# Performance work log

Measured on AMD Instinct MI355X. Metric: run time of the kernel, lower is better.

Reference implementation:

```python
import jax, jax.numpy as jnp
import numpy as np

N = 100000   # nodes
E = 1600000  # edges
D = 128      # in_dim
H = 128      # hidden_dim
C = 40       # num_classes
EPS = 1e-5   # LayerNorm eps (torch default)


def setup_inputs() -> dict:
    key = jax.random.key(0)
    ks = jax.random.split(key, 16)
    x = jax.random.normal(ks[0], (N, D), dtype=jnp.float32)
    edge_index = jax.random.randint(ks[1], (2, E), 0, N, dtype=jnp.int64)
    s = 1.0 / np.sqrt(D)
    inp = {"x": x, "edge_index": edge_index}
    # 3 GCN layers: weight [in, H], bias [H]; LayerNorm gamma/beta [H]
    for i in range(3):
        inp[f"W{i}"] = jax.random.normal(ks[2 + i], (D if i == 0 else H, H), dtype=jnp.float32) * s
        inp[f"b{i}"] = jnp.zeros((H,), jnp.float32)
        inp[f"g{i}"] = jnp.ones((H,), jnp.float32)
        inp[f"be{i}"] = jnp.zeros((H,), jnp.float32)
    inp["Wc"] = jax.random.normal(ks[10], (H, C), dtype=jnp.float32) * (1.0 / np.sqrt(H))
    inp["bc"] = jnp.zeros((C,), jnp.float32)
    return inp


def _layer_norm(h, g, b):
    mu = jnp.mean(h, axis=-1, keepdims=True)
    var = jnp.var(h, axis=-1, keepdims=True)  # biased, matches torch
    return (h - mu) * jax.lax.rsqrt(var + EPS) * g + b


def _gcn_conv(x, W, b, src, dst, enorm, dinv2):
    # GCNConv: D^{-1/2}(A+I)D^{-1/2} X W + b (self-loops handled analytically)
    h = x @ W                                   # [N, H]
    agg = jax.ops.segment_sum(h[src] * enorm[:, None], dst, num_segments=N)
    return agg + h * dinv2[:, None] + b


def reference(x, edge_index, W0, b0, g0, be0, W1, b1, g1, be1, W2, b2, g2, be2, Wc, bc):
    src, dst = edge_index[0], edge_index[1]
    # degree with self-loops (GCNConv adds self-loops by default)
    deg = jnp.zeros((N,), x.dtype).at[dst].add(1.0) + 1.0
    dinv = jax.lax.rsqrt(deg)
    enorm = dinv[src] * dinv[dst]               # per-edge normalization
    dinv2 = dinv * dinv                         # self-loop normalization

    Ws, bs, gs, bes = (W0, W1, W2), (b0, b1, b2), (g0, g1, g2), (be0, be1, be2)
    for i in range(3):
        x_in = x
        x = _gcn_conv(x, Ws[i], bs[i], src, dst, enorm, dinv2)
        x = _layer_norm(x, gs[i], bes[i])
        x = jax.nn.elu(x)
        if i > 0:
            x = x + x_in
        # dropout: eval mode / p=0 -> identity
    return x @ Wc + bc
```

## Files before the change

kernel.cpp:

```cpp
#include <hip/hip_runtime.h>
#include <math.h>

#define N_NODES 100000
#define N_EDGES 1600000
#define DIM     128
#define NCLS    40
#define NBUCK   196
#define P1_CH   4096
#define P1_GRID 391

typedef _Float16 f16x8 __attribute__((ext_vector_type(8)));
typedef _Float16 f16x2 __attribute__((ext_vector_type(2)));
typedef float    f32x4 __attribute__((ext_vector_type(4)));

__device__ inline unsigned short f16bits(float f) {
    union { _Float16 h; unsigned short u; } cv;
    cv.h = (_Float16)f;
    return cv.u;
}
__device__ inline f16x2 as_h2(unsigned u) {
    union { unsigned u; f16x2 h; } cv;
    cv.u = u;
    return cv.h;
}
__device__ inline unsigned as_u(f16x2 h) {
    union { f16x2 h; unsigned u; } cv;
    cv.h = h;
    return cv.u;
}
__device__ inline unsigned pack_h2(float lo, float hi) {
    f16x2 h;
    h.x = (_Float16)lo;
    h.y = (_Float16)hi;
    return as_u(h);
}
__device__ inline int wave_incl_scan(int v, int lane) {
#pragma unroll
    for (int off = 1; off < 64; off <<= 1) {
        int x = __shfl_up(v, off, 64);
        if (lane >= off) v += x;
    }
    return v;
}

__global__ __launch_bounds__(256) void setup_misc(const float* __restrict__ W0,
                                                  const float* __restrict__ W1,
                                                  const float* __restrict__ W2,
                                                  const float* __restrict__ Wc,
                                                  const int* __restrict__ ei,
                                                  unsigned short* __restrict__ Wsw0,
                                                  unsigned short* __restrict__ Wsw1,
                                                  unsigned short* __restrict__ Wsw2,
                                                  unsigned short* __restrict__ Wcsw,
                                                  int* __restrict__ bcnt) {
    int blk = blockIdx.x;
    if (blk < 192) {
        const float* W = (blk < 64) ? W0 : (blk < 128) ? W1 : W2;
        unsigned short* Wsw = (blk < 64) ? Wsw0 : (blk < 128) ? Wsw1 : Wsw2;
        int o = (blk & 63) * 256 + threadIdx.x;
        int f = o >> 9;
        int l = (o >> 3) & 63;
        int j = o & 7;
        int n = f >> 2;
        int s = f & 3;
        int k = s * 32 + (l >> 4) * 8 + j;
        int c = (l & 15) * 8 + n;
        Wsw[o] = f16bits(W[k * DIM + c]);
    } else if (blk < 216) {
        int o = (blk - 192) * 256 + threadIdx.x;
        int f = o >> 9;
        int l = (o >> 3) & 63;
        int j = o & 7;
        int n = f >> 2;
        int s = f & 3;
        int k = s * 32 + (l >> 4) * 8 + j;
        int c = (l & 15) * 3 + n;
        Wcsw[o] = (c < NCLS) ? f16bits(Wc[k * NCLS + c]) : (unsigned short)0;
    } else {
        __shared__ int h[256];
        const int t  = threadIdx.x;
        const int e0 = (blk - 216) * P1_CH;
        const int cnt = min(P1_CH, N_EDGES - e0);
        h[t] = 0;
        __syncthreads();
        for (int i = t; i < cnt; i += 256)
            atomicAdd(&h[ei[N_EDGES + e0 + i] >> 9], 1);
        __syncthreads();
        if (h[t]) atomicAdd(&bcnt[t], h[t]);
    }
}

__global__ __launch_bounds__(256) void bucket_p1(const int* __restrict__ ei,
                                                 const int* __restrict__ bcnt,
                                                 int* __restrict__ boff,
                                                 unsigned* __restrict__ tmp) {
    __shared__ int  hist[256];
    __shared__ int  lscan[256];
    __shared__ int  rank[256];
    __shared__ int  gbase[256];
    __shared__ int  wtotA[4];
    __shared__ int  wtotB[4];
    __shared__ int2 stage[P1_CH];
    const int t  = threadIdx.x;
    const int lane = t & 63, wv = t >> 6;
    const int e0 = blockIdx.x * P1_CH;
    const int cnt = min(P1_CH, N_EDGES - e0);

    int bcv = (t < NBUCK) ? bcnt[t] : 0;

    hist[t] = 0;
    __syncthreads();

    int2 ed[16];
#pragma unroll
    for (int i = 0; i < 16; ++i) {
        int idx = t + i * 256;
        if (idx < cnt) {
            int s = ei[e0 + idx];
            int d = ei[N_EDGES + e0 + idx];
            ed[i] = make_int2(s, d);
            atomicAdd(&hist[d >> 9], 1);
        }
    }
    __syncthreads();

    int hv = hist[t];
    int inclA = hv, inclB = bcv;
#pragma unroll
    for (int off = 1; off < 64; off <<= 1) {
        int xa = __shfl_up(inclA, off, 64);
        int xb = __shfl_up(inclB, off, 64);
        if (lane >= off) { inclA += xa; inclB += xb; }
    }
    if (lane == 63) { wtotA[wv] = inclA; wtotB[wv] = inclB; }
    __syncthreads();
    int pA = 0, pB = 0;
    for (int i = 0; i < wv; ++i) { pA += wtotA[i]; pB += wtotB[i]; }
    inclA += pA;
    inclB += pB;
    int exclA = inclA - hv;
    int exclB = inclB - bcv;
    lscan[t] = exclA;
    rank[t]  = exclA;
    if (hv > 0) gbase[t] = exclB + atomicAdd(&boff[t], hv);
    __syncthreads();

#pragma unroll
    for (int i = 0; i < 16; ++i) {
        int idx = t + i * 256;
        if (idx < cnt) {
            int b = ed[i].y >> 9;
            int p = atomicAdd(&rank[b], 1);
            stage[p] = ed[i];
        }
    }
    __syncthreads();

    for (int p = t; p < cnt; p += 256) {
        int2 v = stage[p];
        int b = v.y >> 9;
        tmp[gbase[b] + (p - lscan[b])] = ((unsigned)v.x << 9) | ((unsigned)v.y & 511u);
    }
}

__global__ __launch_bounds__(256) void bucket_p2(const unsigned* __restrict__ tmp,
                                                 const int* __restrict__ bcnt,
                                                 int* __restrict__ rowptr,
                                                 float* __restrict__ dinv,
                                                 unsigned* __restrict__ rec) {
    __shared__ int cnt[512];
    __shared__ int cur[512];
    __shared__ int wtot[4];
    __shared__ int sbeg, send;
    const int t  = threadIdx.x;
    const int lane = t & 63, wv = t >> 6;
    const int b  = blockIdx.x;
    const int d0 = b << 9;
    const int dend = min(d0 + 512, N_NODES);
    const int nn = dend - d0;

    int bcv = (t < NBUCK) ? bcnt[t] : 0;
    int binc = wave_incl_scan(bcv, lane);
    if (lane == 63) wtot[wv] = binc;
    cnt[t] = 0;
    cnt[t + 256] = 0;
    __syncthreads();
    {
        int pfx = 0;
        for (int i = 0; i < wv; ++i) pfx += wtot[i];
        binc += pfx;
        if (t == b) { sbeg = binc - bcv; send = binc; }
    }
    __syncthreads();

    const int beg = sbeg;
    const int end = send;
    for (int idx = beg + t; idx < end; idx += 256)
        atomicAdd(&cnt[tmp[idx] & 511u], 1);
    __syncthreads();

    int c0 = cnt[2 * t];
    int c1 = cnt[2 * t + 1];
    int pv = c0 + c1;
    int incl = wave_incl_scan(pv, lane);
    if (lane == 63) wtot[wv] = incl;
    __syncthreads();
    int prefix = 0;
    for (int i = 0; i < wv; ++i) prefix += wtot[i];
    incl += prefix;
    int excl = incl - pv;
    int base0 = beg + excl;
    int base1 = base0 + c0;
    cur[2 * t]     = base0;
    cur[2 * t + 1] = base1;
    if (2 * t < nn) {
        rowptr[d0 + 2 * t] = base0;
        dinv[d0 + 2 * t]   = rsqrtf((float)c0 + 1.0f);
    }
    if (2 * t + 1 < nn) {
        rowptr[d0 + 2 * t + 1] = base1;
        dinv[d0 + 2 * t + 1]   = rsqrtf((float)c1 + 1.0f);
    }
    if (b == NBUCK - 1 && t == 0) rowptr[N_NODES] = N_EDGES;
    __syncthreads();

    for (int idx = beg + t; idx < end; idx += 256) {
        unsigned u = tmp[idx];
        int pos = atomicAdd(&cur[u & 511u], 1);
        rec[pos] = (u >> 9) << 8;
    }
}

__global__ __launch_bounds__(256) void gemm_mfma_f(const float* __restrict__ X,
                                                   const unsigned short* __restrict__ Wsw,
                                                   const float* __restrict__ dinv,
                                                   unsigned short* __restrict__ H) {
    __shared__ unsigned short wlds[32 * 512];
    const int tid   = threadIdx.x;
    const int lane  = tid & 63;
    const int wave  = tid >> 6;
    const int row0w = blockIdx.x * 64 + wave * 16;
    const int m = lane & 15;
    const int q = lane >> 4;

    {
        const uint4* srcp = (const uint4*)Wsw;
        uint4*       dstp = (uint4*)wlds;
#pragma unroll
        for (int i = 0; i < 8; ++i) dstp[tid + i * 256] = srcp[tid + i * 256];
    }
    __syncthreads();

    int r = row0w + m;
    if (r >= N_NODES) r = N_NODES - 1;
    const float* xp = X + (size_t)r * DIM + q * 8;
    f16x8 af[4];
#pragma unroll
    for (int s = 0; s < 4; ++s) {
        float4 x0 = *(const float4*)(xp + s * 32);
        float4 x1 = *(const float4*)(xp + s * 32 + 4);
        f16x8 v;
        v[0] = (_Float16)x0.x; v[1] = (_Float16)x0.y;
        v[2] = (_Float16)x0.z; v[3] = (_Float16)x0.w;
        v[4] = (_Float16)x1.x; v[5] = (_Float16)x1.y;
        v[6] = (_Float16)x1.z; v[7] = (_Float16)x1.w;
        af[s] = v;
    }

    f32x4 acc[8];
    f32x4 z = {0.f, 0.f, 0.f, 0.f};
#pragma unroll
    for (int n = 0; n < 8; ++n) acc[n] = z;

    const unsigned short* wl = wlds + lane * 8;
#pragma unroll
    for (int s = 0; s < 4; ++s)
#pragma unroll
        for (int n = 0; n < 8; ++n) {
            f16x8 wf = *(const f16x8*)(wl + ((n * 4 + s) << 9));
            acc[n] = __builtin_amdgcn_mfma_f32_16x16x32_f16(af[s], wf, acc[n], 0, 0, 0);
        }

#pragma unroll
    for (int j = 0; j < 4; ++j) {
        int row = row0w + q * 4 + j;
        if (row < N_NODES) {
            float dv = dinv[row];
            uint4 o;
            o.x = pack_h2(acc[0][j] * dv, acc[1][j] * dv);
            o.y = pack_h2(acc[2][j] * dv, acc[3][j] * dv);
            o.z = pack_h2(acc[4][j] * dv, acc[5][j] * dv);
            o.w = pack_h2(acc[6][j] * dv, acc[7][j] * dv);
            *(uint4*)(H + (size_t)row * DIM + m * 8) = o;
        } else {
            uint4 zz = make_uint4(0u, 0u, 0u, 0u);
            *(uint4*)(H + (size_t)row * DIM + m * 8) = zz;
        }
    }
}

__global__ __launch_bounds__(256) void gemm_mfma_h(const unsigned short* __restrict__ Xh,
                                                   const unsigned short* __restrict__ Wsw,
                                                   const float* __restrict__ dinv,
                                                   unsigned short* __restrict__ H) {
    __shared__ unsigned short wlds[32 * 512];
    const int tid   = threadIdx.x;
    const int lane  = tid & 63;
    const int wave  = tid >> 6;
    const int row0w = blockIdx.x * 64 + wave * 16;
    const int m = lane & 15;
    const int q = lane >> 4;

    {
        const uint4* srcp = (const uint4*)Wsw;
        uint4*       dstp = (uint4*)wlds;
#pragma unroll
        for (int i = 0; i < 8; ++i) dstp[tid + i * 256] = srcp[tid + i * 256];
    }
    __syncthreads();

    int r = row0w + m;
    if (r >= N_NODES) r = N_NODES - 1;
    const unsigned short* xp = Xh + (size_t)r * DIM + q * 8;
    f16x8 af[4];
#pragma unroll
    for (int s = 0; s < 4; ++s) af[s] = *(const f16x8*)(xp + s * 32);

    f32x4 acc[8];
    f32x4 z = {0.f, 0.f, 0.f, 0.f};
#pragma unroll
    for (int n = 0; n < 8; ++n) acc[n] = z;

    const unsigned short* wl = wlds + lane * 8;
#pragma unroll
    for (int s = 0; s < 4; ++s)
#pragma unroll
        for (int n = 0; n < 8; ++n) {
            f16x8 wf = *(const f16x8*)(wl + ((n * 4 + s) << 9));
            acc[n] = __builtin_amdgcn_mfma_f32_16x16x32_f16(af[s], wf, acc[n], 0, 0, 0);
        }

#pragma unroll
    for (int j = 0; j < 4; ++j) {
        int row = row0w + q * 4 + j;
        if (row < N_NODES) {
            float dv = dinv[row];
            uint4 o;
            o.x = pack_h2(acc[0][j] * dv, acc[1][j] * dv);
            o.y = pack_h2(acc[2][j] * dv, acc[3][j] * dv);
            o.z = pack_h2(acc[4][j] * dv, acc[5][j] * dv);
            o.w = pack_h2(acc[6][j] * dv, acc[7][j] * dv);
            *(uint4*)(H + (size_t)row * DIM + m * 8) = o;
        } else {
            uint4 zz = make_uint4(0u, 0u, 0u, 0u);
            *(uint4*)(H + (size_t)row * DIM + m * 8) = zz;
        }
    }
}

__global__ __launch_bounds__(256) void agg_ln(const unsigned short* __restrict__ Hh,
                                              const unsigned short* __restrict__ xin,
                                              const float* __restrict__ dinv,
                                              const float* __restrict__ bias,
                                              const float* __restrict__ g,
                                              const float* __restrict__ be,
                                              const int* __restrict__ rowptr,
                                              const unsigned* __restrict__ rec,
                                              unsigned short* __restrict__ outb) {
    const int tid  = threadIdx.x;
    const int lane = tid & 63;
    const int l16  = tid & 15;
    const int gb   = lane & 48;
    const int node = blockIdx.x * 16 + (tid >> 4);
    const int beg  = rowptr[node];
    const int end  = rowptr[node + 1];
    const char* Hb8 = (const char*)Hh;
    const unsigned laneoff = (unsigned)l16 * 16;
    const unsigned sentin  = (unsigned)N_NODES << 8;

    f16x2 accA[4], accB[4], accC[4], accD[4];
    f16x2 hz = {(_Float16)0.f, (_Float16)0.f};
#pragma unroll
    for (int k = 0; k < 4; ++k) { accA[k] = hz; accB[k] = hz; accC[k] = hz; accD[k] = hz; }

    for (int e0 = beg; e0 < end; e0 += 16) {
        int cnt = min(end - e0, 16);
        unsigned sv = (l16 < cnt) ? rec[e0 + l16] : sentin;
        int cntR = (cnt + 7) & ~7;
        for (int j = 0; j < cntR; j += 8) {
            unsigned o0 = (unsigned)__shfl((int)sv, gb + j + 0, 64) + laneoff;
            unsigned o1 = (unsigned)__shfl((int)sv, gb + j + 1, 64) + laneoff;
            unsigned o2 = (unsigned)__shfl((int)sv, gb + j + 2, 64) + laneoff;
            unsigned o3 = (unsigned)__shfl((int)sv, gb + j + 3, 64) + laneoff;
            unsigned o4 = (unsigned)__shfl((int)sv, gb + j + 4, 64) + laneoff;
            unsigned o5 = (unsigned)__shfl((int)sv, gb + j + 5, 64) + laneoff;
            unsigned o6 = (unsigned)__shfl((int)sv, gb + j + 6, 64) + laneoff;
            unsigned o7 = (unsigned)__shfl((int)sv, gb + j + 7, 64) + laneoff;
            uint4 u0 = *(const uint4*)(Hb8 + o0);
            uint4 u1 = *(const uint4*)(Hb8 + o1);
            uint4 u2 = *(const uint4*)(Hb8 + o2);
            uint4 u3 = *(const uint4*)(Hb8 + o3);
            uint4 u4 = *(const uint4*)(Hb8 + o4);
            uint4 u5 = *(const uint4*)(Hb8 + o5);
            uint4 u6 = *(const uint4*)(Hb8 + o6);
            uint4 u7 = *(const uint4*)(Hb8 + o7);
            accA[0] += as_h2(u0.x); accA[1] += as_h2(u0.y); accA[2] += as_h2(u0.z); accA[3] += as_h2(u0.w);
            accB[0] += as_h2(u1.x); accB[1] += as_h2(u1.y); accB[2] += as_h2(u1.z); accB[3] += as_h2(u1.w);
            accC[0] += as_h2(u2.x); accC[1] += as_h2(u2.y); accC[2] += as_h2(u2.z); accC[3] += as_h2(u2.w);
            accD[0] += as_h2(u3.x); accD[1] += as_h2(u3.y); accD[2] += as_h2(u3.z); accD[3] += as_h2(u3.w);
            accA[0] += as_h2(u4.x); accA[1] += as_h2(u4.y); accA[2] += as_h2(u4.z); accA[3] += as_h2(u4.w);
            accB[0] += as_h2(u5.x); accB[1] += as_h2(u5.y); accB[2] += as_h2(u5.z); accB[3] += as_h2(u5.w);
            accC[0] += as_h2(u6.x); accC[1] += as_h2(u6.y); accC[2] += as_h2(u6.z); accC[3] += as_h2(u6.w);
            accD[0] += as_h2(u7.x); accD[1] += as_h2(u7.y); accD[2] += as_h2(u7.z); accD[3] += as_h2(u7.w);
        }
    }

#pragma unroll
    for (int k = 0; k < 4; ++k) accA[k] = (accA[k] + accB[k]) + (accC[k] + accD[k]);

    const float dv = dinv[node];
    const unsigned nodeoff = ((unsigned)node << 8) + laneoff;
    uint4 hv = *(const uint4*)(Hb8 + nodeoff);
    const int c0 = l16 * 8;
    float4 bb0 = *(const float4*)(bias + c0);
    float4 bb1 = *(const float4*)(bias + c0 + 4);
    f16x2 h0 = as_h2(hv.x), h1 = as_h2(hv.y), h2 = as_h2(hv.z), h3 = as_h2(hv.w);

    float a[8];
    a[0] = ((float)accA[0].x + (float)h0.x) * dv + bb0.x;
    a[1] = ((float)accA[0].y + (float)h0.y) * dv + bb0.y;
    a[2] = ((float)accA[1].x + (float)h1.x) * dv + bb0.z;
    a[3] = ((float)accA[1].y + (float)h1.y) * dv + bb0.w;
    a[4] = ((float)accA[2].x + (float)h2.x) * dv + bb1.x;
    a[5] = ((float)accA[2].y + (float)h2.y) * dv + bb1.y;
    a[6] = ((float)accA[3].x + (float)h3.x) * dv + bb1.z;
    a[7] = ((float)accA[3].y + (float)h3.y) * dv + bb1.w;

    float s1 = 0.f, s2 = 0.f;
#pragma unroll
    for (int i = 0; i < 8; ++i) { s1 += a[i]; s2 += a[i] * a[i]; }
#pragma unroll
    for (int mk = 1; mk <= 8; mk <<= 1) {
        s1 += __shfl_xor(s1, mk, 64);
        s2 += __shfl_xor(s2, mk, 64);
    }
    float mean = s1 * (1.0f / 128.0f);
    float var  = s2 * (1.0f / 128.0f) - mean * mean;
    float rr   = rsqrtf(var + 1e-5f);

    float4 gg0 = *(const float4*)(g + c0);
    float4 gg1 = *(const float4*)(g + c0 + 4);
    float4 ee0 = *(const float4*)(be + c0);
    float4 ee1 = *(const float4*)(be + c0 + 4);

    float r[8];
    r[0] = (a[0] - mean) * rr * gg0.x + ee0.x;
    r[1] = (a[1] - mean) * rr * gg0.y + ee0.y;
    r[2] = (a[2] - mean) * rr * gg0.z + ee0.z;
    r[3] = (a[3] - mean) * rr * gg0.w + ee0.w;
    r[4] = (a[4] - mean) * rr * gg1.x + ee1.x;
    r[5] = (a[5] - mean) * rr * gg1.y + ee1.y;
    r[6] = (a[6] - mean) * rr * gg1.z + ee1.z;
    r[7] = (a[7] - mean) * rr * gg1.w + ee1.w;
#pragma unroll
    for (int i = 0; i < 8; ++i) r[i] = r[i] > 0.0f ? r[i] : expm1f(r[i]);

    if (xin) {
        uint4 xv = *(const uint4*)((const char*)xin + nodeoff);
        f16x2 x0 = as_h2(xv.x), x1 = as_h2(xv.y), x2 = as_h2(xv.z), x3 = as_h2(xv.w);
        r[0] += (float)x0.x; r[1] += (float)x0.y;
        r[2] += (float)x1.x; r[3] += (float)x1.y;
        r[4] += (float)x2.x; r[5] += (float)x2.y;
        r[6] += (float)x3.x; r[7] += (float)x3.y;
    }

    uint4 o;
    o.x = pack_h2(r[0], r[1]);
    o.y = pack_h2(r[2], r[3]);
    o.z = pack_h2(r[4], r[5]);
    o.w = pack_h2(r[6], r[7]);
    *(uint4*)((char*)outb + nodeoff) = o;
}

__global__ __launch_bounds__(256) void agg_ln_cls(const unsigned short* __restrict__ Hh,
                                                  const unsigned short* __restrict__ xin,
                                                  const float* __restrict__ dinv,
                                                  const float* __restrict__ bias,
                                                  const float* __restrict__ g,
                                                  const float* __restrict__ be,
                                                  const int* __restrict__ rowptr,
                                                  const unsigned* __restrict__ rec,
                                                  const unsigned short* __restrict__ Wcsw,
                                                  const float* __restrict__ bc,
                                                  float* __restrict__ out) {
    __shared__ _Float16 hl[16][136];
    const int tid  = threadIdx.x;
    const int lane = tid & 63;
    const int l16  = tid & 15;
    const int gb   = lane & 48;
    const int grp  = tid >> 4;
    const int node0 = blockIdx.x * 16;
    const int node = node0 + grp;
    const int beg  = rowptr[node];
    const int end  = rowptr[node + 1];
    const char* Hb8 = (const char*)Hh;
    const unsigned laneoff = (unsigned)l16 * 16;
    const unsigned sentin  = (unsigned)N_NODES << 8;

    f16x2 accA[4], accB[4], accC[4], accD[4];
    f16x2 hz = {(_Float16)0.f, (_Float16)0.f};
#pragma unroll
    for (int k = 0; k < 4; ++k) { accA[k] = hz; accB[k] = hz; accC[k] = hz; accD[k] = hz; }

    for (int e0 = beg; e0 < end; e0 += 16) {
        int cnt = min(end - e0, 16);
        unsigned sv = (l16 < cnt) ? rec[e0 + l16] : sentin;
        int cntR = (cnt + 7) & ~7;
        for (int j = 0; j < cntR; j += 8) {
            unsigned o0 = (unsigned)__shfl((int)sv, gb + j + 0, 64) + laneoff;
            unsigned o1 = (unsigned)__shfl((int)sv, gb + j + 1, 64) + laneoff;
            unsigned o2 = (unsigned)__shfl((int)sv, gb + j + 2, 64) + laneoff;
            unsigned o3 = (unsigned)__shfl((int)sv, gb + j + 3, 64) + laneoff;
            unsigned o4 = (unsigned)__shfl((int)sv, gb + j + 4, 64) + laneoff;
            unsigned o5 = (unsigned)__shfl((int)sv, gb + j + 5, 64) + laneoff;
            unsigned o6 = (unsigned)__shfl((int)sv, gb + j + 6, 64) + laneoff;
            unsigned o7 = (unsigned)__shfl((int)sv, gb + j + 7, 64) + laneoff;
            uint4 u0 = *(const uint4*)(Hb8 + o0);
            uint4 u1 = *(const uint4*)(Hb8 + o1);
            uint4 u2 = *(const uint4*)(Hb8 + o2);
            uint4 u3 = *(const uint4*)(Hb8 + o3);
            uint4 u4 = *(const uint4*)(Hb8 + o4);
            uint4 u5 = *(const uint4*)(Hb8 + o5);
            uint4 u6 = *(const uint4*)(Hb8 + o6);
            uint4 u7 = *(const uint4*)(Hb8 + o7);
            accA[0] += as_h2(u0.x); accA[1] += as_h2(u0.y); accA[2] += as_h2(u0.z); accA[3] += as_h2(u0.w);
            accB[0] += as_h2(u1.x); accB[1] += as_h2(u1.y); accB[2] += as_h2(u1.z); accB[3] += as_h2(u1.w);
            accC[0] += as_h2(u2.x); accC[1] += as_h2(u2.y); accC[2] += as_h2(u2.z); accC[3] += as_h2(u2.w);
            accD[0] += as_h2(u3.x); accD[1] += as_h2(u3.y); accD[2] += as_h2(u3.z); accD[3] += as_h2(u3.w);
            accA[0] += as_h2(u4.x); accA[1] += as_h2(u4.y); accA[2] += as_h2(u4.z); accA[3] += as_h2(u4.w);
            accB[0] += as_h2(u5.x); accB[1] += as_h2(u5.y); accB[2] += as_h2(u5.z); accB[3] += as_h2(u5.w);
            accC[0] += as_h2(u6.x); accC[1] += as_h2(u6.y); accC[2] += as_h2(u6.z); accC[3] += as_h2(u6.w);
            accD[0] += as_h2(u7.x); accD[1] += as_h2(u7.y); accD[2] += as_h2(u7.z); accD[3] += as_h2(u7.w);
        }
    }

#pragma unroll
    for (int k = 0; k < 4; ++k) accA[k] = (accA[k] + accB[k]) + (accC[k] + accD[k]);

    const float dv = dinv[node];
    const unsigned nodeoff = ((unsigned)node << 8) + laneoff;
    uint4 hv = *(const uint4*)(Hb8 + nodeoff);
    const int c0 = l16 * 8;
    float4 bb0 = *(const float4*)(bias + c0);
    float4 bb1 = *(const float4*)(bias + c0 + 4);
    f16x2 h0 = as_h2(hv.x), h1 = as_h2(hv.y), h2 = as_h2(hv.z), h3 = as_h2(hv.w);

    float a[8];
    a[0] = ((float)accA[0].x + (float)h0.x) * dv + bb0.x;
    a[1] = ((float)accA[0].y + (float)h0.y) * dv + bb0.y;
    a[2] = ((float)accA[1].x + (float)h1.x) * dv + bb0.z;
    a[3] = ((float)accA[1].y + (float)h1.y) * dv + bb0.w;
    a[4] = ((float)accA[2].x + (float)h2.x) * dv + bb1.x;
    a[5] = ((float)accA[2].y + (float)h2.y) * dv + bb1.y;
    a[6] = ((float)accA[3].x + (float)h3.x) * dv + bb1.z;
    a[7] = ((float)accA[3].y + (float)h3.y) * dv + bb1.w;

    float s1 = 0.f, s2 = 0.f;
#pragma unroll
    for (int i = 0; i < 8; ++i) { s1 += a[i]; s2 += a[i] * a[i]; }
#pragma unroll
    for (int mk = 1; mk <= 8; mk <<= 1) {
        s1 += __shfl_xor(s1, mk, 64);
        s2 += __shfl_xor(s2, mk, 64);
    }
    float mean = s1 * (1.0f / 128.0f);
    float var  = s2 * (1.0f / 128.0f) - mean * mean;
    float rr   = rsqrtf(var + 1e-5f);

    float4 gg0 = *(const float4*)(g + c0);
    float4 gg1 = *(const float4*)(g + c0 + 4);
    float4 ee0 = *(const float4*)(be + c0);
    float4 ee1 = *(const float4*)(be + c0 + 4);

    float r[8];
    r[0] = (a[0] - mean) * rr * gg0.x + ee0.x;
    r[1] = (a[1] - mean) * rr * gg0.y + ee0.y;
    r[2] = (a[2] - mean) * rr * gg0.z + ee0.z;
    r[3] = (a[3] - mean) * rr * gg0.w + ee0.w;
    r[4] = (a[4] - mean) * rr * gg1.x + ee1.x;
    r[5] = (a[5] - mean) * rr * gg1.y + ee1.y;
    r[6] = (a[6] - mean) * rr * gg1.z + ee1.z;
    r[7] = (a[7] - mean) * rr * gg1.w + ee1.w;
#pragma unroll
    for (int i = 0; i < 8; ++i) r[i] = r[i] > 0.0f ? r[i] : expm1f(r[i]);

    if (xin) {
        uint4 xv = *(const uint4*)((const char*)xin + nodeoff);
        f16x2 x0 = as_h2(xv.x), x1 = as_h2(xv.y), x2 = as_h2(xv.z), x3 = as_h2(xv.w);
        r[0] += (float)x0.x; r[1] += (float)x0.y;
        r[2] += (float)x1.x; r[3] += (float)x1.y;
        r[4] += (float)x2.x; r[5] += (float)x2.y;
        r[6] += (float)x3.x; r[7] += (float)x3.y;
    }

    uint4 o;
    o.x = pack_h2(r[0], r[1]);
    o.y = pack_h2(r[2], r[3]);
    o.z = pack_h2(r[4], r[5]);
    o.w = pack_h2(r[6], r[7]);
    *(uint4*)&hl[grp][l16 * 8] = o;
    __syncthreads();

    if (tid < 64) {
        const int m = lane & 15;
        const int q = lane >> 4;

        f16x8 wf[12];
#pragma unroll
        for (int f = 0; f < 12; ++f)
            wf[f] = *(const f16x8*)(Wcsw + (f << 9) + lane * 8);

        f16x8 af[4];
#pragma unroll
        for (int s = 0; s < 4; ++s)
            af[s] = *(const f16x8*)&hl[m][q * 8 + s * 32];

        f32x4 acc[3];
        f32x4 z = {0.f, 0.f, 0.f, 0.f};
#pragma unroll
        for (int n = 0; n < 3; ++n) acc[n] = z;

#pragma unroll
        for (int s = 0; s < 4; ++s)
#pragma unroll
            for (int n = 0; n < 3; ++n)
                acc[n] = __builtin_amdgcn_mfma_f32_16x16x32_f16(af[s], wf[n * 4 + s], acc[n], 0, 0, 0);

#pragma unroll
        for (int j = 0; j < 4; ++j) {
            int row = node0 + q * 4 + j;
#pragma unroll
            for (int n = 0; n < 3; ++n) {
                int c = 3 * m + n;
                if (c < NCLS)
                    out[(size_t)row * NCLS + c] = acc[n][j] + bc[c];
            }
        }
    }
}

extern "C" void kernel_launch(void* const* d_in, const int* in_sizes, int n_in,
                              void* d_out, int out_size, void* d_ws, size_t ws_size,
                              hipStream_t stream) {
    const float* x  = (const float*)d_in[0];
    const int*   ei = (const int*)d_in[1];
    const float* W[3]  = {(const float*)d_in[2], (const float*)d_in[6], (const float*)d_in[10]};
    const float* b[3]  = {(const float*)d_in[3], (const float*)d_in[7], (const float*)d_in[11]};
    const float* g[3]  = {(const float*)d_in[4], (const float*)d_in[8], (const float*)d_in[12]};
    const float* be[3] = {(const float*)d_in[5], (const float*)d_in[9], (const float*)d_in[13]};
    const float* Wc = (const float*)d_in[14];
    const float* bc = (const float*)d_in[15];
    float* out = (float*)d_out;

    char* ws = (char*)d_ws;
    const size_t NP = 400128;
    float* dinv   = (float*)(ws);
    int*   rowptr = (int*)  (ws + NP);
    int*   bcnt   = (int*)  (ws + 2 * NP);
    int*   boff   = (int*)  (ws + 2 * NP + 1024);
    unsigned* rec = (unsigned*)(ws + 2 * NP + 4096);
    unsigned short* Hh = (unsigned short*)(ws + 2 * NP + 4096 + (size_t)N_EDGES * 8);
    unsigned short* Ah = Hh + (size_t)(N_NODES + 64) * DIM;
    unsigned short* Ch = Ah + (size_t)N_NODES * DIM;
    unsigned short* Wsw0 = Ch + (size_t)N_NODES * DIM;
    unsigned short* Wsw1 = Wsw0 + DIM * DIM;
    unsigned short* Wsw2 = Wsw1 + DIM * DIM;
    unsigned short* Wcsw = Wsw2 + DIM * DIM;
    unsigned* tmp = (unsigned*)Ch;

    hipMemsetAsync(bcnt, 0, 2048, stream);
    setup_misc<<<216 + P1_GRID, 256, 0, stream>>>(W[0], W[1], W[2], Wc, ei,
                                                  Wsw0, Wsw1, Wsw2, Wcsw, bcnt);

    bucket_p1<<<P1_GRID, 256, 0, stream>>>(ei, bcnt, boff, tmp);
    bucket_p2<<<NBUCK, 256, 0, stream>>>(tmp, bcnt, rowptr, dinv, rec);

    const int gemm_grid = (N_NODES + 63) / 64;
    const int agg_grid  = N_NODES / 16;

    gemm_mfma_f<<<gemm_grid, 256, 0, stream>>>(x, Wsw0, dinv, Hh);
    agg_ln<<<agg_grid, 256, 0, stream>>>(Hh, nullptr, dinv, b[0], g[0], be[0], rowptr, rec, Ch);

    gemm_mfma_h<<<gemm_grid, 256, 0, stream>>>(Ch, Wsw1, dinv, Hh);
    agg_ln<<<agg_grid, 256, 0, stream>>>(Hh, Ch, dinv, b[1], g[1], be[1], rowptr, rec, Ah);

    gemm_mfma_h<<<gemm_grid, 256, 0, stream>>>(Ah, Wsw2, dinv, Hh);
    agg_ln_cls<<<agg_grid, 256, 0, stream>>>(Hh, Ah, dinv, b[2], g[2], be[2], rowptr, rec,
                                             Wcsw, bc, out);
}
```

Before: 389.4 us.

## Fuse next-layer GEMM into aggregation+LayerNorm kernel epilogue

Replaces the separate gemm_mfma_h launches by computing each block's 16 output rows times the next layer weight inside the aggregation kernel, via LDS staging and MFMA with weights read directly from global memory. The aim is to avoid re-reading the layer activations from HBM and to save two kernel launches. H is double-buffered (H1/H2) because aggregation gathers from arbitrary rows, and the padding rows of H2 are zeroed in setup. The residual input and the output buffer Ch are now aliased across the two fused layers, and each wave writes strided 4-byte stores, which could hurt coalescing.

Result: faster. 372.2 us (-4.4%).

```diff
diff --git a/kernel.cpp b/kernel.cpp
--- a/kernel.cpp
+++ b/kernel.cpp
@@ -52,7 +52,8 @@
                                                   unsigned short* __restrict__ Wsw1,
                                                   unsigned short* __restrict__ Wsw2,
                                                   unsigned short* __restrict__ Wcsw,
-                                                  int* __restrict__ bcnt) {
+                                                  int* __restrict__ bcnt,
+                                                  unsigned short* __restrict__ H2) {
     int blk = blockIdx.x;
     if (blk < 192) {
         const float* W = (blk < 64) ? W0 : (blk < 128) ? W1 : W2;
@@ -76,7 +77,7 @@
         int k = s * 32 + (l >> 4) * 8 + j;
         int c = (l & 15) * 3 + n;
         Wcsw[o] = (c < NCLS) ? f16bits(Wc[k * NCLS + c]) : (unsigned short)0;
-    } else {
+    } else if (blk < 216 + P1_GRID) {
         __shared__ int h[256];
         const int t  = threadIdx.x;
         const int e0 = (blk - 216) * P1_CH;
@@ -87,6 +88,11 @@
             atomicAdd(&h[ei[N_EDGES + e0 + i] >> 9], 1);
         __syncthreads();
         if (h[t]) atomicAdd(&bcnt[t], h[t]);
+    } else {
+        uint4* p = (uint4*)(H2 + (size_t)N_NODES * DIM);
+        uint4 zz = make_uint4(0u, 0u, 0u, 0u);
+#pragma unroll
+        for (int i = 0; i < 4; ++i) p[threadIdx.x + i * 256] = zz;
     }
 }
 
@@ -299,79 +305,26 @@
     }
 }
 
-__global__ __launch_bounds__(256) void gemm_mfma_h(const unsigned short* __restrict__ Xh,
+__global__ __launch_bounds__(256) void agg_ln_gemm(const unsigned short* __restrict__ Hh,
+                                                   const unsigned short* __restrict__ xin,
+                                                   const float* __restrict__ dinv,
+                                                   const float* __restrict__ bias,
+                                                   const float* __restrict__ g,
+                                                   const float* __restrict__ be,
+                                                   const int* __restrict__ rowptr,
+                                                   const unsigned* __restrict__ rec,
                                                    const unsigned short* __restrict__ Wsw,
-                                                   const float* __restrict__ dinv,
-                                                   unsigned short* __restrict__ H) {
-    __shared__ unsigned short wlds[32 * 512];
-    const int tid   = threadIdx.x;
-    const int lane  = tid & 63;
-    const int wave  = tid >> 6;
-    const int row0w = blockIdx.x * 64 + wave * 16;
-    const int m = lane & 15;
-    const int q = lane >> 4;
-
-    {
-        const uint4* srcp = (const uint4*)Wsw;
-        uint4*       dstp = (uint4*)wlds;
-#pragma unroll
-        for (int i = 0; i < 8; ++i) dstp[tid + i * 256] = srcp[tid + i * 256];
-    }
-    __syncthreads();
-
-    int r = row0w + m;
-    if (r >= N_NODES) r = N_NODES - 1;
-    const unsigned short* xp = Xh + (size_t)r * DIM + q * 8;
-    f16x8 af[4];
-#pragma unroll
-    for (int s = 0; s < 4; ++s) af[s] = *(const f16x8*)(xp + s * 32);
-
-    f32x4 acc[8];
-    f32x4 z = {0.f, 0.f, 0.f, 0.f};
-#pragma unroll
-    for (int n = 0; n < 8; ++n) acc[n] = z;
-
-    const unsigned short* wl = wlds + lane * 8;
-#pragma unroll
-    for (int s = 0; s < 4; ++s)
-#pragma unroll
-        for (int n = 0; n < 8; ++n) {
-            f16x8 wf = *(const f16x8*)(wl + ((n * 4 + s) << 9));
-            acc[n] = __builtin_amdgcn_mfma_f32_16x16x32_f16(af[s], wf, acc[n], 0, 0, 0);
-        }
-
-#pragma unroll
-    for (int j = 0; j < 4; ++j) {
-        int row = row0w + q * 4 + j;
-        if (row < N_NODES) {
-            float dv = dinv[row];
-            uint4 o;
-            o.x = pack_h2(acc[0][j] * dv, acc[1][j] * dv);
-            o.y = pack_h2(acc[2][j] * dv, acc[3][j] * dv);
-            o.z = pack_h2(acc[4][j] * dv, acc[5][j] * dv);
-            o.w = pack_h2(acc[6][j] * dv, acc[7][j] * dv);
-            *(uint4*)(H + (size_t)row * DIM + m * 8) = o;
-        } else {
-            uint4 zz = make_uint4(0u, 0u, 0u, 0u);
-            *(uint4*)(H + (size_t)row * DIM + m * 8) = zz;
-        }
-    }
-}
-
-__global__ __launch_bounds__(256) void agg_ln(const unsigned short* __restrict__ Hh,
-                                              const unsigned short* __restrict__ xin,
-                                              const float* __restrict__ dinv,
-                                              const float* __restrict__ bias,
-                                              const float* __restrict__ g,
-                                              const float* __restrict__ be,
-                                              const int* __restrict__ rowptr,
-                                              const unsigned* __restrict__ rec,
-                                              unsigned short* __restrict__ outb) {
+                                                   unsigned short* __restrict__ Cout,
+                                                   unsigned short* __restrict__ Hout) {
+    __shared__ _Float16 hl[16][136];
     const int tid  = threadIdx.x;
     const int lane = tid & 63;
     const int l16  = tid & 15;
     const int gb   = lane & 48;
-    const int node = blockIdx.x * 16 + (tid >> 4);
+    const int grp  = tid >> 4;
+    const int wave = tid >> 6;
+    const int node0 = blockIdx.x * 16;
+    const int node = node0 + grp;
     const int beg  = rowptr[node];
     const int end  = rowptr[node + 1];
     const char* Hb8 = (const char*)Hh;
@@ -479,7 +432,39 @@
     o.y = pack_h2(r[2], r[3]);
     o.z = pack_h2(r[4], r[5]);
     o.w = pack_h2(r[6], r[7]);
-    *(uint4*)((char*)outb + nodeoff) = o;
+    *(uint4*)((char*)Cout + nodeoff) = o;
+    *(uint4*)&hl[grp][l16 * 8] = o;
+    __syncthreads();
+
+    {
+        const int m = lane & 15;
+        const int q = lane >> 4;
+
+        f16x8 af[4];
+#pragma unroll
+        for (int s = 0; s < 4; ++s)
+            af[s] = *(const f16x8*)&hl[m][q * 8 + s * 32];
+
+        f32x4 acc2[2];
+        f32x4 z = {0.f, 0.f, 0.f, 0.f};
+        acc2[0] = z; acc2[1] = z;
+
+#pragma unroll
+        for (int s = 0; s < 4; ++s)
+#pragma unroll
+            for (int p = 0; p < 2; ++p) {
+                f16x8 wfv = *(const f16x8*)(Wsw + (((2 * wave + p) * 4 + s) << 9) + lane * 8);
+                acc2[p] = __builtin_amdgcn_mfma_f32_16x16x32_f16(af[s], wfv, acc2[p], 0, 0, 0);
+            }
+
+#pragma unroll
+        for (int j = 0; j < 4; ++j) {
+            int row = node0 + q * 4 + j;
+            float dv2 = dinv[row];
+            *(unsigned*)((char*)Hout + ((unsigned)row << 8) + ((unsigned)(m * 8 + 2 * wave) << 1)) =
+                pack_h2(acc2[0][j] * dv2, acc2[1][j] * dv2);
+        }
+    }
 }
 
 __global__ __launch_bounds__(256) void agg_ln_cls(const unsigned short* __restrict__ Hh,
@@ -669,9 +654,9 @@
     int*   bcnt   = (int*)  (ws + 2 * NP);
     int*   boff   = (int*)  (ws + 2 * NP + 1024);
     unsigned* rec = (unsigned*)(ws + 2 * NP + 4096);
-    unsigned short* Hh = (unsigned short*)(ws + 2 * NP + 4096 + (size_t)N_EDGES * 8);
-    unsigned short* Ah = Hh + (size_t)(N_NODES + 64) * DIM;
-    unsigned short* Ch = Ah + (size_t)N_NODES * DIM;
+    unsigned short* H1 = (unsigned short*)(ws + 2 * NP + 4096 + (size_t)N_EDGES * 8);
+    unsigned short* H2 = H1 + (size_t)(N_NODES + 64) * DIM;
+    unsigned short* Ch = H2 + (size_t)(N_NODES + 64) * DIM;
     unsigned short* Wsw0 = Ch + (size_t)N_NODES * DIM;
     unsigned short* Wsw1 = Wsw0 + DIM * DIM;
     unsigned short* Wsw2 = Wsw1 + DIM * DIM;
@@ -679,8 +664,8 @@
     unsigned* tmp = (unsigned*)Ch;
 
     hipMemsetAsync(bcnt, 0, 2048, stream);
-    setup_misc<<<216 + P1_GRID, 256, 0, stream>>>(W[0], W[1], W[2], Wc, ei,
-                                                  Wsw0, Wsw1, Wsw2, Wcsw, bcnt);
+    setup_misc<<<216 + P1_GRID + 1, 256, 0, stream>>>(W[0], W[1], W[2], Wc, ei,
+                                                      Wsw0, Wsw1, Wsw2, Wcsw, bcnt, H2);
 
     bucket_p1<<<P1_GRID, 256, 0, stream>>>(ei, bcnt, boff, tmp);
     bucket_p2<<<NBUCK, 256, 0, stream>>>(tmp, bcnt, rowptr, dinv, rec);
@@ -688,13 +673,14 @@
     const int gemm_grid = (N_NODES + 63) / 64;
     const int agg_grid  = N_NODES / 16;
 
-    gemm_mfma_f<<<gemm_grid, 256, 0, stream>>>(x, Wsw0, dinv, Hh);
-    agg_ln<<<agg_grid, 256, 0, stream>>>(Hh, nullptr, dinv, b[0], g[0], be[0], rowptr, rec, Ch);
-
-    gemm_mfma_h<<<gemm_grid, 256, 0, stream>>>(Ch, Wsw1, dinv, Hh);
-    agg_ln<<<agg_grid, 256, 0, stream>>>(Hh, Ch, dinv, b[1], g[1], be[1], rowptr, rec, Ah);
-
-    gemm_mfma_h<<<gemm_grid, 256, 0, stream>>>(Ah, Wsw2, dinv, Hh);
-    agg_ln_cls<<<agg_grid, 256, 0, stream>>>(Hh, Ah, dinv, b[2], g[2], be[2], rowptr, rec,
-                                             Wcsw, bc, out);
-}
+    gemm_mfma_f<<<gemm_grid, 256, 0, stream>>>(x, Wsw0, dinv, H1);
+
+    agg_ln_gemm<<<agg_grid, 256, 0, stream>>>(H1, nullptr, dinv, b[0], g[0], be[0],
+                                              rowptr, rec, Wsw1, Ch, H2);
+
+    agg_ln_gemm<<<agg_grid, 256, 0, stream>>>(H2, Ch, dinv, b[1], g[1], be[1],
+                                              rowptr, rec, Wsw2, Ch, H1);
+
+    agg_ln_cls<<<agg_grid, 256, 0, stream>>>(H1, Ch, dinv, b[2], g[2], be[2],
+                                             rowptr, rec, Wcsw, bc, out);
+}
```
